# Performance work log

Hardware: AMD Instinct MI355X
Metric: run time of the kernel (lower is better)

## Reference

```python
import jax, jax.numpy as jnp
import numpy as np

WINDOW = 11
SIGMA = 1.5
CHANNELS = 3
C1 = 0.01 ** 2
C2 = 0.03 ** 2


def _gaussian_kernel(size=WINDOW, sigma=SIGMA, channels=CHANNELS):
    coords = jnp.arange(size, dtype=jnp.float32) - size // 2
    g = jnp.exp(-coords ** 2 / (2.0 * sigma ** 2))
    g = jnp.outer(g, g)
    g = g / g.sum()
    # depthwise kernel: [C, 1, K, K] (OIHW with feature_group_count=C)
    return jnp.broadcast_to(g[None, None], (channels, 1, size, size))


def _dwconv(x, kernel):
    # x: [N, C, H, W]; SAME padding, depthwise (groups = C)
    pad = WINDOW // 2
    return jax.lax.conv_general_dilated(
        x, kernel,
        window_strides=(1, 1),
        padding=[(pad, pad), (pad, pad)],
        dimension_numbers=('NCHW', 'OIHW', 'NCHW'),
        feature_group_count=CHANNELS,
    )


def setup_inputs() -> dict:
    key = jax.random.key(0)
    k1, k2 = jax.random.split(key)
    shape = (16, 3, 512, 512)
    pred = jax.random.uniform(k1, shape, dtype=jnp.float32)
    target = jax.random.uniform(k2, shape, dtype=jnp.float32)
    return {"pred": pred, "target": target}


def reference(pred, target):
    kernel = _gaussian_kernel().astype(pred.dtype)
    mu_p = _dwconv(pred, kernel)
    mu_t = _dwconv(target, kernel)
    mu_p2 = mu_p * mu_p
    mu_t2 = mu_t * mu_t
    mu_pt = mu_p * mu_t
    sigma_p2 = _dwconv(pred * pred, kernel) - mu_p2
    sigma_t2 = _dwconv(target * target, kernel) - mu_t2
    sigma_pt = _dwconv(pred * target, kernel) - mu_pt
    ssim_map = ((2.0 * mu_pt + C1) * (2.0 * sigma_pt + C2)) / (
        (mu_p2 + mu_t2 + C1) * (sigma_p2 + sigma_t2 + C2)
    )
    return 1.0 - ssim_map.mean()
```

## Files before the change

kernel.cpp:

```cpp
#include <hip/hip_runtime.h>
#include <math.h>

#define IMG_H 512
#define IMG_W 512
#define NSLOT 64

typedef _Float16 f16x4 __attribute__((ext_vector_type(4)));
typedef _Float16 f16x8 __attribute__((ext_vector_type(8)));
typedef float    f32x4 __attribute__((ext_vector_type(4)));

__device__ const _Float16 WPAD[52] = {
    (_Float16)0.f,(_Float16)0.f,(_Float16)0.f,(_Float16)0.f,(_Float16)0.f,(_Float16)0.f,
    (_Float16)0.f,(_Float16)0.f,(_Float16)0.f,(_Float16)0.f,(_Float16)0.f,(_Float16)0.f,
    (_Float16)0.f,(_Float16)0.f,(_Float16)0.f,(_Float16)0.f,(_Float16)0.f,(_Float16)0.f,
    (_Float16)0.00102838f, (_Float16)0.00759876f, (_Float16)0.03600077f,
    (_Float16)0.10936065f, (_Float16)0.21300554f, (_Float16)0.26601173f,
    (_Float16)0.21300554f, (_Float16)0.10936065f, (_Float16)0.03600077f,
    (_Float16)0.00759876f, (_Float16)0.00102838f,
    (_Float16)0.f,(_Float16)0.f,(_Float16)0.f,(_Float16)0.f,(_Float16)0.f,(_Float16)0.f,
    (_Float16)0.f,(_Float16)0.f,(_Float16)0.f,(_Float16)0.f,(_Float16)0.f,(_Float16)0.f,
    (_Float16)0.f,(_Float16)0.f,(_Float16)0.f,(_Float16)0.f,(_Float16)0.f,(_Float16)0.f,
    (_Float16)0.f,(_Float16)0.f,(_Float16)0.f,(_Float16)0.f,(_Float16)0.f
};

__device__ __forceinline__ f16x8 frag_from_tab(int base)
{
    f16x8 f;
    #pragma unroll
    for (int j = 0; j < 8; ++j) f[j] = WPAD[base + j];
    return f;
}

#define HT_BYTES (4 * 4 * 16 * 48 * 2)

__global__ __launch_bounds__(256, 6)
void ssim_main(const float* __restrict__ pred, const float* __restrict__ targ,
               float* __restrict__ partial, double* __restrict__ acc, int mode)
{
    __shared__ __align__(128) _Float16 hT[4][4][16][48];

    const int tid  = threadIdx.x;
    const int lane = tid & 63, wave = tid >> 6;
    const int ln   = lane & 15, lg = lane >> 4;

    const int bid   = ((blockIdx.z * 16 + blockIdx.y) * 8) + blockIdx.x;
    const int chunk = (int)gridDim.z << 4;
    const int nb    = (bid & 7) * chunk + (bid >> 3);
    const int img   = nb >> 7;
    const int rem   = nb & 127;
    const int ty    = rem >> 3, tx = rem & 7;

    const float* __restrict__ p = pred + (size_t)img * (IMG_H * IMG_W);
    const float* __restrict__ t = targ + (size_t)img * (IMG_H * IMG_W);

    const int gr0 = ty * 32 - 5;
    const int wo  = tx * 64 + wave * 16 - 8;

    const f16x8 Bw  = frag_from_tab(15 + lg * 8 - ln);
    const f16x8 A2w = frag_from_tab(18 + lg * 8 - ln);
    const f32x4 z = {0.f, 0.f, 0.f, 0.f};

    const int  gc    = wo + lg * 8;
    const bool colOK = (gc >= 0) && (gc <= IMG_W - 8);
    const int  gcc   = gc < 0 ? 0 : (gc > IMG_W - 8 ? IMG_W - 8 : gc);

    int  grr[3]; bool ok[3];
    const float *bp[3], *bt[3];
    #pragma unroll
    for (int rt = 0; rt < 3; ++rt) {
        const int gr = gr0 + rt * 16 + ln;
        ok[rt] = ((unsigned)gr < (unsigned)IMG_H) && colOK;
        const int grc = gr < 0 ? 0 : (gr > IMG_H - 1 ? IMG_H - 1 : gr);
        grr[rt] = grc;
        bp[rt] = p + (size_t)grc * IMG_W + gcc;
        bt[rt] = t + (size_t)grc * IMG_W + gcc;
    }

    const int swz = (ln & 4) << 2;

    auto proc = [&](int rt, float4 a0, float4 a1, float4 b0, float4 b1, bool in) {
        const _Float16 mh = in ? (_Float16)1.0f : (_Float16)0.0f;
        const f16x8 mv = {mh, mh, mh, mh, mh, mh, mh, mh};
        f16x8 s8 = f16x8{
            (_Float16)(a0.x + b0.x), (_Float16)(a0.y + b0.y),
            (_Float16)(a0.z + b0.z), (_Float16)(a0.w + b0.w),
            (_Float16)(a1.x + b1.x), (_Float16)(a1.y + b1.y),
            (_Float16)(a1.z + b1.z), (_Float16)(a1.w + b1.w)} * mv;
        f16x8 d8 = f16x8{
            (_Float16)(a0.x - b0.x), (_Float16)(a0.y - b0.y),
            (_Float16)(a0.z - b0.z), (_Float16)(a0.w - b0.w),
            (_Float16)(a1.x - b1.x), (_Float16)(a1.y - b1.y),
            (_Float16)(a1.z - b1.z), (_Float16)(a1.w - b1.w)} * mv;
        f16x8 fq[4];
        fq[0] = s8; fq[1] = d8;
        fq[2] = s8 * s8; fq[3] = d8 * d8;
        const int woff = ((rt * 16 + lg * 4) * 2) ^ swz;
        #pragma unroll
        for (int q = 0; q < 4; ++q) {
            f32x4 dd = __builtin_amdgcn_mfma_f32_16x16x32_f16(fq[q], Bw, z, 0, 0, 0);
            *(f16x4*)((char*)&hT[wave][q][ln][0] + woff) =
                f16x4{(_Float16)dd[0], (_Float16)dd[1], (_Float16)dd[2], (_Float16)dd[3]};
        }
    };

    float4 a00 = ((const float4*)bp[0])[0], a01 = ((const float4*)bp[0])[1];
    float4 b00 = ((const float4*)bt[0])[0], b01 = ((const float4*)bt[0])[1];
    float4 a10 = ((const float4*)bp[1])[0], a11 = ((const float4*)bp[1])[1];
    float4 b10 = ((const float4*)bt[1])[0], b11 = ((const float4*)bt[1])[1];
    proc(0, a00, a01, b00, b01, ok[0]);
    float4 a20 = ((const float4*)bp[2])[0], a21 = ((const float4*)bp[2])[1];
    float4 b20 = ((const float4*)bt[2])[0], b21 = ((const float4*)bt[2])[1];
    proc(1, a10, a11, b10, b11, ok[1]);
    proc(2, a20, a21, b20, b21, ok[2]);

    asm volatile("s_waitcnt lgkmcnt(0)" ::: "memory");
    __builtin_amdgcn_sched_barrier(0);

    float lsum = 0.f;
    const float C1 = 1e-4f, C2 = 9e-4f;
    #pragma unroll
    for (int v = 0; v < 2; ++v) {
        const int roff = ((v * 16 + lg * 8) * 2) ^ swz;
        f32x4 accq[4];
        #pragma unroll
        for (int q = 0; q < 4; ++q) {
            f16x8 b = *(const f16x8*)((char*)&hT[wave][q][ln][0] + roff);
            accq[q] = __builtin_amdgcn_mfma_f32_16x16x32_f16(A2w, b, z, 0, 0, 0);
        }
        #pragma unroll
        for (int r = 0; r < 4; ++r) {
            float F1 = accq[0][r], F2 = accq[1][r];
            float F3 = accq[2][r], F4 = accq[3][r];
            float a = F1 * F1, b = F2 * F2;
            float mpmt2 = 0.5f * (a - b);
            float msq   = 0.5f * (a + b);
            float cpt2  = 0.5f * (F3 - F4) - mpmt2;
            float vsum  = 0.5f * (F3 + F4) - msq;
            float num = (mpmt2 + C1) * (cpt2 + C2);
            float den = (msq + C1) * (vsum + C2);
            lsum = fmaf(num, __builtin_amdgcn_rcpf(den), lsum);
        }
    }

    #pragma unroll
    for (int off = 32; off > 0; off >>= 1)
        lsum += __shfl_down(lsum, off, 64);
    if (lane == 0) {
        if (mode == 0) partial[nb * 4 + wave] = lsum;
        else atomicAdd(&acc[(nb * 4 + wave) & (NSLOT - 1)], (double)lsum);
    }
}

__global__ void ssim_init(double* acc)
{
    if (threadIdx.x < NSLOT) acc[threadIdx.x] = 0.0;
}

__global__ __launch_bounds__(1024)
void ssim_fin_slots(const float* __restrict__ partial, float* __restrict__ out,
                    int n4, double inv_n)
{
    __shared__ double red[16];
    double s = 0.0;
    const int tid = threadIdx.x;
    for (int i = tid; i < n4; i += 1024) {
        float4 v = ((const float4*)partial)[i];
        s += (double)v.x + (double)v.y + (double)v.z + (double)v.w;
    }
    #pragma unroll
    for (int off = 32; off > 0; off >>= 1)
        s += __shfl_down(s, off, 64);
    if ((tid & 63) == 0) red[tid >> 6] = s;
    __syncthreads();
    if (tid == 0) {
        double tot = 0.0;
        #pragma unroll
        for (int w = 0; w < 16; ++w) tot += red[w];
        out[0] = (float)(1.0 - tot * inv_n);
    }
}

__global__ void ssim_fin_atomic(const double* __restrict__ acc, float* __restrict__ out,
                                double inv_n)
{
    if (threadIdx.x == 0) {
        double s = 0.0;
        for (int i = 0; i < NSLOT; ++i) s += acc[i];
        out[0] = (float)(1.0 - s * inv_n);
    }
}

extern "C" void kernel_launch(void* const* d_in, const int* in_sizes, int n_in,
                              void* d_out, int out_size, void* d_ws, size_t ws_size,
                              hipStream_t stream)
{
    const float* pred = (const float*)d_in[0];
    const float* targ = (const float*)d_in[1];
    float* out = (float*)d_out;

    const long long total = (long long)in_sizes[0];
    const int n_img = (int)(total / (IMG_H * IMG_W));
    dim3 grid(IMG_W / 64, IMG_H / 32, n_img);
    const int nblk = grid.x * grid.y * grid.z;
    const int nslots = nblk * 4;
    const double inv_n = 1.0 / (double)total;

    if (ws_size >= (size_t)nslots * sizeof(float)) {
        float* partial = (float*)d_ws;
        hipLaunchKernelGGL(ssim_main, grid, dim3(256), 0, stream,
                           pred, targ, partial, (double*)nullptr, 0);
        hipLaunchKernelGGL(ssim_fin_slots, dim3(1), dim3(1024), 0, stream,
                           partial, out, nslots / 4, inv_n);
    } else {
        double* acc = (double*)d_ws;
        hipLaunchKernelGGL(ssim_init, dim3(1), dim3(64), 0, stream, acc);
        hipLaunchKernelGGL(ssim_main, grid, dim3(256), 0, stream,
                           pred, targ, (float*)nullptr, acc, 1);
        hipLaunchKernelGGL(ssim_fin_atomic, dim3(1), dim3(1), 0, stream,
                           acc, out, inv_n);
    }
}
```

Before: 141.1 us.

## Loop each block over four row tiles with software-pipelined prefetch

Each block now walks four consecutive 32-row tiles (128 rows) instead of one, and the grid shrinks fourfold. The global loads for the next tile's first two row groups are issued while the current tile's MFMA and LDS work runs, so memory latency overlaps compute. The aim is to cut per-block launch and setup overhead and hide load latency in a latency-bound kernel. In exchange there are fewer blocks to spread over the CUs, and the overlapping halo row group is still reloaded each iteration rather than reused.

```diff
diff --git a/kernel.cpp b/kernel.cpp
--- a/kernel.cpp
+++ b/kernel.cpp
@@ -31,8 +31,6 @@
     return f;
 }
 
-#define HT_BYTES (4 * 4 * 16 * 48 * 2)
-
 __global__ __launch_bounds__(256, 6)
 void ssim_main(const float* __restrict__ pred, const float* __restrict__ targ,
                float* __restrict__ partial, double* __restrict__ acc, int mode)
@@ -43,40 +41,37 @@
     const int lane = tid & 63, wave = tid >> 6;
     const int ln   = lane & 15, lg = lane >> 4;
 
-    const int bid   = ((blockIdx.z * 16 + blockIdx.y) * 8) + blockIdx.x;
-    const int chunk = (int)gridDim.z << 4;
-    const int nb    = (bid & 7) * chunk + (bid >> 3);
-    const int img   = nb >> 7;
-    const int rem   = nb & 127;
-    const int ty    = rem >> 3, tx = rem & 7;
+    const int bid   = ((blockIdx.z * 4 + blockIdx.y) * 8) + blockIdx.x;
+    const int chunk = (int)gridDim.z * 4;
+    const int nbk   = (bid & 7) * chunk + (bid >> 3);
+    const int img   = nbk >> 5;
+    const int rem   = nbk & 31;
+    const int tygrp = rem >> 3, tx = rem & 7;
 
     const float* __restrict__ p = pred + (size_t)img * (IMG_H * IMG_W);
     const float* __restrict__ t = targ + (size_t)img * (IMG_H * IMG_W);
-
-    const int gr0 = ty * 32 - 5;
-    const int wo  = tx * 64 + wave * 16 - 8;
 
     const f16x8 Bw  = frag_from_tab(15 + lg * 8 - ln);
     const f16x8 A2w = frag_from_tab(18 + lg * 8 - ln);
     const f32x4 z = {0.f, 0.f, 0.f, 0.f};
 
+    const int  wo    = tx * 64 + wave * 16 - 8;
     const int  gc    = wo + lg * 8;
     const bool colOK = (gc >= 0) && (gc <= IMG_W - 8);
     const int  gcc   = gc < 0 ? 0 : (gc > IMG_W - 8 ? IMG_W - 8 : gc);
 
-    int  grr[3]; bool ok[3];
-    const float *bp[3], *bt[3];
-    #pragma unroll
-    for (int rt = 0; rt < 3; ++rt) {
-        const int gr = gr0 + rt * 16 + ln;
-        ok[rt] = ((unsigned)gr < (unsigned)IMG_H) && colOK;
+    const int swz = (ln & 4) << 2;
+
+    auto load_tile = [&](int it, int rt, float4& x0, float4& x1,
+                         float4& y0, float4& y1) -> bool {
+        const int gr  = (tygrp * 4 + it) * 32 - 5 + rt * 16 + ln;
         const int grc = gr < 0 ? 0 : (gr > IMG_H - 1 ? IMG_H - 1 : gr);
-        grr[rt] = grc;
-        bp[rt] = p + (size_t)grc * IMG_W + gcc;
-        bt[rt] = t + (size_t)grc * IMG_W + gcc;
-    }
-
-    const int swz = (ln & 4) << 2;
+        const float* rp = p + (size_t)grc * IMG_W + gcc;
+        const float* rq = t + (size_t)grc * IMG_W + gcc;
+        x0 = ((const float4*)rp)[0]; x1 = ((const float4*)rp)[1];
+        y0 = ((const float4*)rq)[0]; y1 = ((const float4*)rq)[1];
+        return ((unsigned)gr < (unsigned)IMG_H) && colOK;
+    };
 
     auto proc = [&](int rt, float4 a0, float4 a1, float4 b0, float4 b1, bool in) {
         const _Float16 mh = in ? (_Float16)1.0f : (_Float16)0.0f;
@@ -103,42 +98,53 @@
         }
     };
 
-    float4 a00 = ((const float4*)bp[0])[0], a01 = ((const float4*)bp[0])[1];
-    float4 b00 = ((const float4*)bt[0])[0], b01 = ((const float4*)bt[0])[1];
-    float4 a10 = ((const float4*)bp[1])[0], a11 = ((const float4*)bp[1])[1];
-    float4 b10 = ((const float4*)bt[1])[0], b11 = ((const float4*)bt[1])[1];
-    proc(0, a00, a01, b00, b01, ok[0]);
-    float4 a20 = ((const float4*)bp[2])[0], a21 = ((const float4*)bp[2])[1];
-    float4 b20 = ((const float4*)bt[2])[0], b21 = ((const float4*)bt[2])[1];
-    proc(1, a10, a11, b10, b11, ok[1]);
-    proc(2, a20, a21, b20, b21, ok[2]);
-
-    asm volatile("s_waitcnt lgkmcnt(0)" ::: "memory");
-    __builtin_amdgcn_sched_barrier(0);
+    float4 a00, a01, b00, b01, a10, a11, b10, b11;
+    bool ok0 = load_tile(0, 0, a00, a01, b00, b01);
+    bool ok1 = load_tile(0, 1, a10, a11, b10, b11);
 
     float lsum = 0.f;
     const float C1 = 1e-4f, C2 = 9e-4f;
-    #pragma unroll
-    for (int v = 0; v < 2; ++v) {
-        const int roff = ((v * 16 + lg * 8) * 2) ^ swz;
-        f32x4 accq[4];
+
+    #pragma unroll 1
+    for (int it = 0; it < 4; ++it) {
+        float4 a20, a21, b20, b21;
+        const bool ok2 = load_tile(it, 2, a20, a21, b20, b21);
+
+        proc(0, a00, a01, b00, b01, ok0);
+        proc(1, a10, a11, b10, b11, ok1);
+
+        if (it < 3) {
+            ok0 = load_tile(it + 1, 0, a00, a01, b00, b01);
+            ok1 = load_tile(it + 1, 1, a10, a11, b10, b11);
+        }
+
+        proc(2, a20, a21, b20, b21, ok2);
+
+        asm volatile("s_waitcnt lgkmcnt(0)" ::: "memory");
+        __builtin_amdgcn_sched_barrier(0);
+
         #pragma unroll
-        for (int q = 0; q < 4; ++q) {
-            f16x8 b = *(const f16x8*)((char*)&hT[wave][q][ln][0] + roff);
-            accq[q] = __builtin_amdgcn_mfma_f32_16x16x32_f16(A2w, b, z, 0, 0, 0);
-        }
-        #pragma unroll
-        for (int r = 0; r < 4; ++r) {
-            float F1 = accq[0][r], F2 = accq[1][r];
-            float F3 = accq[2][r], F4 = accq[3][r];
-            float a = F1 * F1, b = F2 * F2;
-            float mpmt2 = 0.5f * (a - b);
-            float msq   = 0.5f * (a + b);
-            float cpt2  = 0.5f * (F3 - F4) - mpmt2;
-            float vsum  = 0.5f * (F3 + F4) - msq;
-            float num = (mpmt2 + C1) * (cpt2 + C2);
-            float den = (msq + C1) * (vsum + C2);
-            lsum = fmaf(num, __builtin_amdgcn_rcpf(den), lsum);
+        for (int v = 0; v < 2; ++v) {
+            const int roff = ((v * 16 + lg * 8) * 2) ^ swz;
+            f32x4 accq[4];
+            #pragma unroll
+            for (int q = 0; q < 4; ++q) {
+                f16x8 b = *(const f16x8*)((char*)&hT[wave][q][ln][0] + roff);
+                accq[q] = __builtin_amdgcn_mfma_f32_16x16x32_f16(A2w, b, z, 0, 0, 0);
+            }
+            #pragma unroll
+            for (int r = 0; r < 4; ++r) {
+                float F1 = accq[0][r], F2 = accq[1][r];
+                float F3 = accq[2][r], F4 = accq[3][r];
+                float a = F1 * F1, bb = F2 * F2;
+                float mpmt2 = 0.5f * (a - bb);
+                float msq   = 0.5f * (a + bb);
+                float cpt2  = 0.5f * (F3 - F4) - mpmt2;
+                float vsum  = 0.5f * (F3 + F4) - msq;
+                float num = (mpmt2 + C1) * (cpt2 + C2);
+                float den = (msq + C1) * (vsum + C2);
+                lsum = fmaf(num, __builtin_amdgcn_rcpf(den), lsum);
+            }
         }
     }
 
@@ -146,8 +152,8 @@
     for (int off = 32; off > 0; off >>= 1)
         lsum += __shfl_down(lsum, off, 64);
     if (lane == 0) {
-        if (mode == 0) partial[nb * 4 + wave] = lsum;
-        else atomicAdd(&acc[(nb * 4 + wave) & (NSLOT - 1)], (double)lsum);
+        if (mode == 0) partial[nbk * 4 + wave] = lsum;
+        else atomicAdd(&acc[(nbk * 4 + wave) & (NSLOT - 1)], (double)lsum);
     }
 }
 
@@ -200,7 +206,7 @@
 
     const long long total = (long long)in_sizes[0];
     const int n_img = (int)(total / (IMG_H * IMG_W));
-    dim3 grid(IMG_W / 64, IMG_H / 32, n_img);
+    dim3 grid(IMG_W / 64, IMG_H / 128, n_img);
     const int nblk = grid.x * grid.y * grid.z;
     const int nslots = nblk * 4;
     const double inv_n = 1.0 / (double)total;
```

Result: no change. 142.1 us (+0.7%).

## Coalesce global loads with row-major lane mapping and LDS transpose staging

Applied to the files above, without the earlier changes.

Global loads are remapped so each group of 8 lanes reads one row's 128 contiguous bytes, instead of each lane reading 32 bytes from a different row. The fp16 sum and difference values are then written to a per-wave LDS staging buffer and read back in the layout the MFMA fragments expect. All six row loads are issued up front, and occupancy in launch bounds is lowered from 6 to 4 blocks per CU. The aim is better memory coalescing and more loads in flight, at the cost of extra LDS traffic, more registers, and fewer resident blocks.

```diff
diff --git a/kernel.cpp b/kernel.cpp
--- a/kernel.cpp
+++ b/kernel.cpp
@@ -4,10 +4,13 @@
 #define IMG_H 512
 #define IMG_W 512
 #define NSLOT 64
-
+#define STG_P 56
+
+typedef _Float16 f16x2 __attribute__((ext_vector_type(2)));
 typedef _Float16 f16x4 __attribute__((ext_vector_type(4)));
 typedef _Float16 f16x8 __attribute__((ext_vector_type(8)));
 typedef float    f32x4 __attribute__((ext_vector_type(4)));
+typedef unsigned int uint;
 
 __device__ const _Float16 WPAD[52] = {
     (_Float16)0.f,(_Float16)0.f,(_Float16)0.f,(_Float16)0.f,(_Float16)0.f,(_Float16)0.f,
@@ -31,17 +34,17 @@
     return f;
 }
 
-#define HT_BYTES (4 * 4 * 16 * 48 * 2)
-
-__global__ __launch_bounds__(256, 6)
+__global__ __launch_bounds__(256, 4)
 void ssim_main(const float* __restrict__ pred, const float* __restrict__ targ,
                float* __restrict__ partial, double* __restrict__ acc, int mode)
 {
+    __shared__ __align__(128) _Float16 stg[4][2][16][STG_P];
     __shared__ __align__(128) _Float16 hT[4][4][16][48];
 
     const int tid  = threadIdx.x;
     const int lane = tid & 63, wave = tid >> 6;
     const int ln   = lane & 15, lg = lane >> 4;
+    const int l8   = lane >> 3, l7 = lane & 7;
 
     const int bid   = ((blockIdx.z * 16 + blockIdx.y) * 8) + blockIdx.x;
     const int chunk = (int)gridDim.z << 4;
@@ -60,37 +63,45 @@
     const f16x8 A2w = frag_from_tab(18 + lg * 8 - ln);
     const f32x4 z = {0.f, 0.f, 0.f, 0.f};
 
-    const int  gc    = wo + lg * 8;
-    const bool colOK = (gc >= 0) && (gc <= IMG_W - 8);
-    const int  gcc   = gc < 0 ? 0 : (gc > IMG_W - 8 ? IMG_W - 8 : gc);
-
-    int  grr[3]; bool ok[3];
-    const float *bp[3], *bt[3];
+    const int  cb    = wo * 4 + l7 * 16;
+    const int  cbc   = cb < 0 ? 0 : (cb > 2032 ? 2032 : cb);
+    const bool colOK = (cb == cbc);
+
+    uint2 sp[6], dp[6];
+    #pragma unroll
+    for (int i = 0; i < 6; ++i) {
+        const int gr  = gr0 + i * 8 + l8;
+        const int grc = gr < 0 ? 0 : (gr > IMG_H - 1 ? IMG_H - 1 : gr);
+        const char* rp = (const char*)p + (size_t)grc * (IMG_W * 4) + cbc;
+        const char* rq = (const char*)t + (size_t)grc * (IMG_W * 4) + cbc;
+        float4 pv = *(const float4*)rp;
+        float4 tv = *(const float4*)rq;
+        const bool ok = ((unsigned)gr < (unsigned)IMG_H) && colOK;
+        f16x2 s01 = {(_Float16)(pv.x + tv.x), (_Float16)(pv.y + tv.y)};
+        f16x2 s23 = {(_Float16)(pv.z + tv.z), (_Float16)(pv.w + tv.w)};
+        f16x2 d01 = {(_Float16)(pv.x - tv.x), (_Float16)(pv.y - tv.y)};
+        f16x2 d23 = {(_Float16)(pv.z - tv.z), (_Float16)(pv.w - tv.w)};
+        uint2 sv = {__builtin_bit_cast(uint, s01), __builtin_bit_cast(uint, s23)};
+        uint2 dv = {__builtin_bit_cast(uint, d01), __builtin_bit_cast(uint, d23)};
+        const uint2 zz = {0u, 0u};
+        sp[i] = ok ? sv : zz;
+        dp[i] = ok ? dv : zz;
+    }
+
+    char* stgS = (char*)&stg[wave][0][0][0];
+    char* stgD = (char*)&stg[wave][1][0][0];
+    const int wB  = l8 * 112 + l7 * 8;
+    const int rB  = ln * 112 + lg * 16;
+    const int swz = (ln & 4) << 2;
+
     #pragma unroll
     for (int rt = 0; rt < 3; ++rt) {
-        const int gr = gr0 + rt * 16 + ln;
-        ok[rt] = ((unsigned)gr < (unsigned)IMG_H) && colOK;
-        const int grc = gr < 0 ? 0 : (gr > IMG_H - 1 ? IMG_H - 1 : gr);
-        grr[rt] = grc;
-        bp[rt] = p + (size_t)grc * IMG_W + gcc;
-        bt[rt] = t + (size_t)grc * IMG_W + gcc;
-    }
-
-    const int swz = (ln & 4) << 2;
-
-    auto proc = [&](int rt, float4 a0, float4 a1, float4 b0, float4 b1, bool in) {
-        const _Float16 mh = in ? (_Float16)1.0f : (_Float16)0.0f;
-        const f16x8 mv = {mh, mh, mh, mh, mh, mh, mh, mh};
-        f16x8 s8 = f16x8{
-            (_Float16)(a0.x + b0.x), (_Float16)(a0.y + b0.y),
-            (_Float16)(a0.z + b0.z), (_Float16)(a0.w + b0.w),
-            (_Float16)(a1.x + b1.x), (_Float16)(a1.y + b1.y),
-            (_Float16)(a1.z + b1.z), (_Float16)(a1.w + b1.w)} * mv;
-        f16x8 d8 = f16x8{
-            (_Float16)(a0.x - b0.x), (_Float16)(a0.y - b0.y),
-            (_Float16)(a0.z - b0.z), (_Float16)(a0.w - b0.w),
-            (_Float16)(a1.x - b1.x), (_Float16)(a1.y - b1.y),
-            (_Float16)(a1.z - b1.z), (_Float16)(a1.w - b1.w)} * mv;
+        *(uint2*)(stgS + wB)       = sp[2 * rt];
+        *(uint2*)(stgS + wB + 896) = sp[2 * rt + 1];
+        *(uint2*)(stgD + wB)       = dp[2 * rt];
+        *(uint2*)(stgD + wB + 896) = dp[2 * rt + 1];
+        f16x8 s8 = *(const f16x8*)(stgS + rB);
+        f16x8 d8 = *(const f16x8*)(stgD + rB);
         f16x8 fq[4];
         fq[0] = s8; fq[1] = d8;
         fq[2] = s8 * s8; fq[3] = d8 * d8;
@@ -101,17 +112,7 @@
             *(f16x4*)((char*)&hT[wave][q][ln][0] + woff) =
                 f16x4{(_Float16)dd[0], (_Float16)dd[1], (_Float16)dd[2], (_Float16)dd[3]};
         }
-    };
-
-    float4 a00 = ((const float4*)bp[0])[0], a01 = ((const float4*)bp[0])[1];
-    float4 b00 = ((const float4*)bt[0])[0], b01 = ((const float4*)bt[0])[1];
-    float4 a10 = ((const float4*)bp[1])[0], a11 = ((const float4*)bp[1])[1];
-    float4 b10 = ((const float4*)bt[1])[0], b11 = ((const float4*)bt[1])[1];
-    proc(0, a00, a01, b00, b01, ok[0]);
-    float4 a20 = ((const float4*)bp[2])[0], a21 = ((const float4*)bp[2])[1];
-    float4 b20 = ((const float4*)bt[2])[0], b21 = ((const float4*)bt[2])[1];
-    proc(1, a10, a11, b10, b11, ok[1]);
-    proc(2, a20, a21, b20, b21, ok[2]);
+    }
 
     asm volatile("s_waitcnt lgkmcnt(0)" ::: "memory");
     __builtin_amdgcn_sched_barrier(0);
@@ -131,9 +132,9 @@
         for (int r = 0; r < 4; ++r) {
             float F1 = accq[0][r], F2 = accq[1][r];
             float F3 = accq[2][r], F4 = accq[3][r];
-            float a = F1 * F1, b = F2 * F2;
-            float mpmt2 = 0.5f * (a - b);
-            float msq   = 0.5f * (a + b);
+            float a = F1 * F1, bb = F2 * F2;
+            float mpmt2 = 0.5f * (a - bb);
+            float msq   = 0.5f * (a + bb);
             float cpt2  = 0.5f * (F3 - F4) - mpmt2;
             float vsum  = 0.5f * (F3 + F4) - msq;
             float num = (mpmt2 + C1) * (cpt2 + C2);
```

After: 130.4 us. 1.08x faster.
